# Performance work log

Measured on AMD Instinct MI355X. Metric: run time of the kernel, lower is better.

## Reference

```python
import jax, jax.numpy as jnp
import numpy as np

D_MODEL = 128
NHEAD = 8
HEAD_DIM = D_MODEL // NHEAD  # 16
NUM_LAYERS = 7
NUM_LABELS = 2
N_NODES = 10000
N_EDGES = 160000
NEG_SLOPE = 0.2  # GATv2Conv default negative_slope


def setup_inputs() -> dict:
    key = jax.random.key(0)
    ks = jax.random.split(key, 10)
    s = 1.0 / np.sqrt(D_MODEL)
    inp = {}
    inp["x"] = jax.random.normal(ks[0], (N_NODES, D_MODEL), dtype=jnp.float32)
    inp["edge_index"] = jax.random.randint(ks[1], (2, N_EDGES), 0, N_NODES, dtype=jnp.int64)
    inp["nchunks"] = 8  # uniform extra chunk size -> chunk = NUM_LABELS + 8 = 10
    # per-layer GATv2 params, stacked on a leading layer axis
    inp["Wl"] = jax.random.normal(ks[2], (NUM_LAYERS, D_MODEL, NHEAD * HEAD_DIM), dtype=jnp.float32) * s
    inp["bl"] = jnp.zeros((NUM_LAYERS, NHEAD * HEAD_DIM), dtype=jnp.float32)
    inp["Wr"] = jax.random.normal(ks[3], (NUM_LAYERS, D_MODEL, NHEAD * HEAD_DIM), dtype=jnp.float32) * s
    inp["br"] = jnp.zeros((NUM_LAYERS, NHEAD * HEAD_DIM), dtype=jnp.float32)
    inp["att"] = jax.random.normal(ks[4], (NUM_LAYERS, NHEAD, HEAD_DIM), dtype=jnp.float32) * s
    inp["bias"] = jnp.zeros((NUM_LAYERS, NHEAD * HEAD_DIM), dtype=jnp.float32)
    # split head: Linear(d_model, 1)
    inp["w_head"] = jax.random.normal(ks[5], (D_MODEL, 1), dtype=jnp.float32) * s
    inp["b_head"] = jnp.zeros((1,), dtype=jnp.float32)
    return inp


def _gatv2_layer(x, src, dst, Wl, bl, Wr, br, att, bias):
    # GATv2: e_ij = a^T LeakyReLU(W_l x_j + W_r x_i); alpha = segment-softmax over dst; out_i = sum alpha * W_l x_j
    N = x.shape[0]
    xl = (x @ Wl + bl).reshape(N, NHEAD, HEAD_DIM)
    xr = (x @ Wr + br).reshape(N, NHEAD, HEAD_DIM)
    z = jax.nn.leaky_relu(xl[src] + xr[dst], NEG_SLOPE)          # [E, H, D]
    e = jnp.einsum('ehd,hd->eh', z, att)                          # [E, H]
    emax = jax.ops.segment_max(e, dst, num_segments=N)            # [N, H]
    ex = jnp.exp(e - emax[dst])
    denom = jax.ops.segment_sum(ex, dst, num_segments=N)          # [N, H]
    alpha = ex / (denom[dst] + 1e-16)                             # [E, H]
    out = jax.ops.segment_sum(alpha[..., None] * xl[src], dst, num_segments=N)  # [N, H, D]
    return out.reshape(N, NHEAD * HEAD_DIM) + bias


def reference(x, edge_index, nchunks, Wl, bl, Wr, br, att, bias, w_head, b_head):
    N = x.shape[0]
    loop = jnp.arange(N, dtype=edge_index.dtype)  # GATv2Conv add_self_loops=True
    src = jnp.concatenate([edge_index[0], loop])
    dst = jnp.concatenate([edge_index[1], loop])
    for i in range(NUM_LAYERS):
        x = _gatv2_layer(x, src, dst, Wl[i], bl[i], Wr[i], br[i], att[i], bias[i])
    # uniform split of size (NUM_LABELS + nchunks); keep first NUM_LABELS rows of each chunk
    chunk = NUM_LABELS + int(nchunks)
    xs = x.reshape(-1, chunk, D_MODEL)[:, :NUM_LABELS]            # [n_chunks, num_labels, d]
    out = (xs @ w_head + b_head)[..., 0]                          # [n_chunks, num_labels]
    return out
```

## Files before the change

kernel.cpp:

```cpp
#include <hip/hip_runtime.h>
#include <math.h>

#define NT 256

typedef __attribute__((ext_vector_type(8))) short bf16x8;
typedef __attribute__((ext_vector_type(4))) float f32x4;


__device__ inline int detect_is64(const int* __restrict__ ei) {
    int is64 = 1;
#pragma unroll
    for (int k = 1; k < 16; k += 2) is64 &= (ei[k] == 0);
    return is64;
}

__device__ inline void split1(float f, short& hi, short& lo) {
    unsigned u = __float_as_uint(f);
    hi = (short)(u >> 16);
    float fl = f - __uint_as_float(u & 0xffff0000u);
    lo = (short)(__float_as_uint(fl) >> 16);
}

__device__ inline void cvt8(const float4& a, const float4& b, bf16x8& hi, bf16x8& lo) {
    float f[8] = {a.x, a.y, a.z, a.w, b.x, b.y, b.z, b.w};
#pragma unroll
    for (int j = 0; j < 8; j++) {
        unsigned u = __float_as_uint(f[j]);
        hi[j] = (short)(u >> 16);
        float fl = f[j] - __uint_as_float(u & 0xffff0000u);
        lo[j] = (short)(__float_as_uint(fl) >> 16);
    }
}


__global__ void count_kernel(const int* __restrict__ ei, int E, int N, int* __restrict__ deg) {
    int e = blockIdx.x * blockDim.x + threadIdx.x;
    if (e >= E) return;
    int is64 = detect_is64(ei);
    long long pos = (long long)E + e;
    int d = ei[is64 ? 2 * pos : pos];
    if ((unsigned)d < (unsigned)N) atomicAdd(&deg[d], 1);
}

__global__ __launch_bounds__(1024) void scan_kernel(const int* __restrict__ deg,
                                                    int* __restrict__ off,
                                                    int* __restrict__ cur, int N) {
    __shared__ int wsum[16];
    int t = threadIdx.x;
    int per = (N + 1023) >> 10;
    int b0 = t * per;
    int s = 0;
    for (int k = 0; k < per; k++) {
        int idx = b0 + k;
        if (idx < N) s += deg[idx];
    }
    int lane = t & 63, w = t >> 6;
    int v = s;
#pragma unroll
    for (int o = 1; o < 64; o <<= 1) {
        int u = __shfl_up(v, o, 64);
        if (lane >= o) v += u;
    }
    if (lane == 63) wsum[w] = v;
    __syncthreads();
    if (t == 0) {
        int r = 0;
#pragma unroll
        for (int j = 0; j < 16; j++) { int xx = wsum[j]; wsum[j] = r; r += xx; }
        off[N] = r;
    }
    __syncthreads();
    int run = v - s + wsum[w];
    for (int k = 0; k < per; k++) {
        int idx = b0 + k;
        if (idx < N) {
            off[idx] = run;
            cur[idx] = run;
            run += deg[idx];
        }
    }
}

__global__ void fill_kernel(const int* __restrict__ ei, int E, int N,
                            int* __restrict__ cur, int* __restrict__ esrc) {
    int e = blockIdx.x * blockDim.x + threadIdx.x;
    if (e >= E) return;
    int is64 = detect_is64(ei);
    long long spos = e, dpos = (long long)E + e;
    int s = ei[is64 ? 2 * spos : spos];
    int d = ei[is64 ? 2 * dpos : dpos];
    if ((unsigned)d >= (unsigned)N || (unsigned)s >= (unsigned)N) return;
    int p = atomicAdd(&cur[d], 1);
    esrc[p] = s;
}


__global__ __launch_bounds__(256) void prep_w(const float* __restrict__ Wl,
                                              const float* __restrict__ Wr,
                                              short* __restrict__ Whi,
                                              short* __restrict__ Wlo) {
    __shared__ float Wt[128][17];
    int l = blockIdx.x >> 4;
    int tile = blockIdx.x & 15;
    int c0 = tile * 16;
    const float* Wsrc = (c0 < 128) ? Wl + (size_t)l * 16384 : Wr + (size_t)l * 16384;
    int cbase = (c0 < 128) ? c0 : c0 - 128;
    int t = threadIdx.x;
#pragma unroll
    for (int it = 0; it < 8; it++) {
        int idx = it * 256 + t;
        int k = idx >> 4, c = idx & 15;
        Wt[k][c] = Wsrc[(size_t)k * 128 + cbase + c];
    }
    __syncthreads();
    int kt = t >> 6, lane = t & 63, q = (lane >> 4), cl = lane & 15;
    bf16x8 hi, lo;
#pragma unroll
    for (int j = 0; j < 8; j++) {
        short h, lw;
        split1(Wt[kt * 32 + q * 8 + j][cl], h, lw);
        hi[j] = h; lo[j] = lw;
    }
    size_t off = ((((size_t)l * 16 + tile) * 4 + kt) * 64 + lane) * 8;
    *(bf16x8*)(Whi + off) = hi;
    *(bf16x8*)(Wlo + off) = lo;
}


__global__ __launch_bounds__(256) void cvt_x(const float4* __restrict__ x4,
                                             short* __restrict__ hi,
                                             short* __restrict__ lo, int n8) {
    int id = blockIdx.x * 256 + threadIdx.x;
    if (id >= n8) return;
    float4 a = x4[2 * id];
    float4 b = x4[2 * id + 1];
    bf16x8 h, lw;
    cvt8(a, b, h, lw);
    *(bf16x8*)(hi + (size_t)id * 8) = h;
    *(bf16x8*)(lo + (size_t)id * 8) = lw;
}


__global__ __launch_bounds__(512, 1) void gemm_xlxr(const short* __restrict__ xhi,
                                                    const short* __restrict__ xlo,
                                                    const short* __restrict__ WhiL,
                                                    const short* __restrict__ WloL,
                                                    const float* __restrict__ blv,
                                                    const float* __restrict__ brv,
                                                    float* __restrict__ xl,
                                                    float* __restrict__ xr,
                                                    int N, int ntiles) {
    int t = threadIdx.x;
    int w = t >> 6, lane = t & 63, q = lane >> 4, cl = lane & 15;

    bf16x8 Bh[2][4], Bl[2][4];
    float biasv[2];
    float* outp[2];
    int colc[2];
#pragma unroll
    for (int nt = 0; nt < 2; nt++) {
        int tile = w * 2 + nt;
        int col = tile * 16 + cl;
        if (col < 128) { biasv[nt] = blv[col]; outp[nt] = xl; colc[nt] = col; }
        else           { biasv[nt] = brv[col - 128]; outp[nt] = xr; colc[nt] = col - 128; }
#pragma unroll
        for (int kt = 0; kt < 4; kt++) {
            size_t off = (((size_t)tile * 4 + kt) * 64 + lane) * 8;
            Bh[nt][kt] = *(const bf16x8*)(WhiL + off);
            Bl[nt][kt] = *(const bf16x8*)(WloL + off);
        }
    }

    int rt = blockIdx.x;
    if (rt >= ntiles) return;
    bf16x8 curH[4], curL[4], nxtH[4], nxtL[4];
    {
        int row = rt * 16 + cl;
        if (row >= N) row = N - 1;
        const short* ph = xhi + (size_t)row * 128 + q * 8;
        const short* pl = xlo + (size_t)row * 128 + q * 8;
#pragma unroll
        for (int kt = 0; kt < 4; kt++) {
            curH[kt] = *(const bf16x8*)(ph + kt * 32);
            curL[kt] = *(const bf16x8*)(pl + kt * 32);
        }
    }

    for (; rt < ntiles; rt += gridDim.x) {
        int rn = rt + gridDim.x;
        if (rn < ntiles) {
            int row = rn * 16 + cl;
            if (row >= N) row = N - 1;
            const short* ph = xhi + (size_t)row * 128 + q * 8;
            const short* pl = xlo + (size_t)row * 128 + q * 8;
#pragma unroll
            for (int kt = 0; kt < 4; kt++) {
                nxtH[kt] = *(const bf16x8*)(ph + kt * 32);
                nxtL[kt] = *(const bf16x8*)(pl + kt * 32);
            }
        }

        f32x4 acc0 = {0.f, 0.f, 0.f, 0.f}, acc1 = {0.f, 0.f, 0.f, 0.f};
#pragma unroll
        for (int kt = 0; kt < 4; kt++) {
            acc0 = __builtin_amdgcn_mfma_f32_16x16x32_bf16(curH[kt], Bh[0][kt], acc0, 0, 0, 0);
            acc1 = __builtin_amdgcn_mfma_f32_16x16x32_bf16(curH[kt], Bh[1][kt], acc1, 0, 0, 0);
            acc0 = __builtin_amdgcn_mfma_f32_16x16x32_bf16(curL[kt], Bh[0][kt], acc0, 0, 0, 0);
            acc1 = __builtin_amdgcn_mfma_f32_16x16x32_bf16(curL[kt], Bh[1][kt], acc1, 0, 0, 0);
            acc0 = __builtin_amdgcn_mfma_f32_16x16x32_bf16(curH[kt], Bl[0][kt], acc0, 0, 0, 0);
            acc1 = __builtin_amdgcn_mfma_f32_16x16x32_bf16(curH[kt], Bl[1][kt], acc1, 0, 0, 0);
        }

#pragma unroll
        for (int nt = 0; nt < 2; nt++) {
            f32x4 a = nt ? acc1 : acc0;
#pragma unroll
            for (int r = 0; r < 4; r++) {
                int row = rt * 16 + q * 4 + r;
                if (row < N) outp[nt][(size_t)row * 128 + colc[nt]] = a[r] + biasv[nt];
            }
        }
#pragma unroll
        for (int kt = 0; kt < 4; kt++) {
            curH[kt] = nxtH[kt];
            curL[kt] = nxtL[kt];
        }
    }
}


__global__ __launch_bounds__(256) void gat_agg(const float4* __restrict__ xl4,
                                               const float4* __restrict__ xr4,
                                               const int* __restrict__ off,
                                               const int* __restrict__ esrc,
                                               const float4* __restrict__ att4,
                                               const float4* __restrict__ bias4,
                                               float4* __restrict__ out4,
                                               short* __restrict__ nhi,
                                               short* __restrict__ nlo, int N) {
    int lane = threadIdx.x & 63;
    int sub = lane >> 4;
    int cl = lane & 15;
    int i = blockIdx.x * 4 + (threadIdx.x >> 6);
    if (i >= N) return;

    float4 xrA = xr4[(size_t)i * 32 + 2 * cl];
    float4 xrB = xr4[(size_t)i * 32 + 2 * cl + 1];
    float4 atA = att4[2 * cl];
    float4 atB = att4[2 * cl + 1];
    int start = off[i];
    int total = off[i + 1] - start + 1;
    int groups = (total + 3) >> 2;

    int k0 = sub;
    int s0 = (k0 < total) ? ((k0 == 0) ? i : esrc[start + k0 - 1]) : i;
    int k1 = 4 + sub;
    int s1 = (k1 < total) ? esrc[start + k1 - 1] : i;
    float4 v0A = xl4[(size_t)s0 * 32 + 2 * cl];
    float4 v0B = xl4[(size_t)s0 * 32 + 2 * cl + 1];
    int k2 = 8 + sub;
    int s2 = (k2 < total) ? esrc[start + k2 - 1] : i;
    float4 v1A = xl4[(size_t)s1 * 32 + 2 * cl];
    float4 v1B = xl4[(size_t)s1 * 32 + 2 * cl + 1];

    float s = 0.f;
    float4 aA = make_float4(0.f, 0.f, 0.f, 0.f);
    float4 aB = make_float4(0.f, 0.f, 0.f, 0.f);

    for (int g = 0; g < groups; g++) {
        int k3 = 4 * (g + 3) + sub;
        int s3 = (k3 < total) ? esrc[start + k3 - 1] : i;
        float4 v2A = xl4[(size_t)s2 * 32 + 2 * cl];
        float4 v2B = xl4[(size_t)s2 * 32 + 2 * cl + 1];

        int kc = 4 * g + sub;
        int valid = kc < total;
        float z0 = v0A.x + xrA.x, z1 = v0A.y + xrA.y, z2 = v0A.z + xrA.z, z3 = v0A.w + xrA.w;
        float z4 = v0B.x + xrB.x, z5 = v0B.y + xrB.y, z6 = v0B.z + xrB.z, z7 = v0B.w + xrB.w;
        z0 = (z0 > 0.f) ? z0 : 0.2f * z0;
        z1 = (z1 > 0.f) ? z1 : 0.2f * z1;
        z2 = (z2 > 0.f) ? z2 : 0.2f * z2;
        z3 = (z3 > 0.f) ? z3 : 0.2f * z3;
        z4 = (z4 > 0.f) ? z4 : 0.2f * z4;
        z5 = (z5 > 0.f) ? z5 : 0.2f * z5;
        z6 = (z6 > 0.f) ? z6 : 0.2f * z6;
        z7 = (z7 > 0.f) ? z7 : 0.2f * z7;
        float p = z0 * atA.x + z1 * atA.y + z2 * atA.z + z3 * atA.w
                + z4 * atB.x + z5 * atB.y + z6 * atB.z + z7 * atB.w;
        p += __shfl_xor(p, 1, 64);
        p = fminf(fmaxf(p, -80.f), 80.f);
        float wgt = valid ? __expf(p) : 0.f;
        s += wgt;
        aA.x += wgt * v0A.x; aA.y += wgt * v0A.y; aA.z += wgt * v0A.z; aA.w += wgt * v0A.w;
        aB.x += wgt * v0B.x; aB.y += wgt * v0B.y; aB.z += wgt * v0B.z; aB.w += wgt * v0B.w;

        v0A = v1A; v0B = v1B;
        v1A = v2A; v1B = v2B;
        s2 = s3;
    }

#pragma unroll
    for (int o = 16; o <= 32; o <<= 1) {
        s += __shfl_xor(s, o, 64);
        aA.x += __shfl_xor(aA.x, o, 64); aA.y += __shfl_xor(aA.y, o, 64);
        aA.z += __shfl_xor(aA.z, o, 64); aA.w += __shfl_xor(aA.w, o, 64);
        aB.x += __shfl_xor(aB.x, o, 64); aB.y += __shfl_xor(aB.y, o, 64);
        aB.z += __shfl_xor(aB.z, o, 64); aB.w += __shfl_xor(aB.w, o, 64);
    }
    if (sub == 0) {
        float inv = 1.f / (s + 1e-16f);
        float4 bA = bias4[2 * cl], bB = bias4[2 * cl + 1];
        float4 oA, oB;
        oA.x = aA.x * inv + bA.x; oA.y = aA.y * inv + bA.y;
        oA.z = aA.z * inv + bA.z; oA.w = aA.w * inv + bA.w;
        oB.x = aB.x * inv + bB.x; oB.y = aB.y * inv + bB.y;
        oB.z = aB.z * inv + bB.z; oB.w = aB.w * inv + bB.w;
        out4[(size_t)i * 32 + 2 * cl] = oA;
        out4[(size_t)i * 32 + 2 * cl + 1] = oB;
        if (nhi) {
            bf16x8 h, lw;
            cvt8(oA, oB, h, lw);
            *(bf16x8*)(nhi + (size_t)i * 128 + cl * 8) = h;
            *(bf16x8*)(nlo + (size_t)i * 128 + cl * 8) = lw;
        }
    }
}


__global__ __launch_bounds__(128) void head_kernel(const float* __restrict__ x,
                                                   const float* __restrict__ w,
                                                   const float* __restrict__ bh,
                                                   const int* __restrict__ nch,
                                                   float* __restrict__ out) {
    __shared__ float r[2];
    int b = blockIdx.x, t = threadIdx.x;
    int chunk = 2 + nch[0];
    int row = (b >> 1) * chunk + (b & 1);
    float p = x[(size_t)row * 128 + t] * w[t];
#pragma unroll
    for (int o = 32; o >= 1; o >>= 1) p += __shfl_xor(p, o, 64);
    if ((t & 63) == 0) r[t >> 6] = p;
    __syncthreads();
    if (t == 0) out[b] = r[0] + r[1] + bh[0];
}


extern "C" void kernel_launch(void* const* d_in, const int* in_sizes, int n_in,
                              void* d_out, int out_size, void* d_ws, size_t ws_size,
                              hipStream_t stream) {
    const float* x0 = (const float*)d_in[0];
    const int* ei = (const int*)d_in[1];
    const int* nchunks = (const int*)d_in[2];
    const float* Wl = (const float*)d_in[3];
    const float* bl = (const float*)d_in[4];
    const float* Wr = (const float*)d_in[5];
    const float* br = (const float*)d_in[6];
    const float* att = (const float*)d_in[7];
    const float* bias = (const float*)d_in[8];
    const float* wh = (const float*)d_in[9];
    const float* bh = (const float*)d_in[10];

    const int D = 128;
    int N = in_sizes[0] / D;
    int E = in_sizes[1] / 2;
    int ntiles = (N + 15) / 16;

    size_t fN = (size_t)N * D;
    const size_t WFRAG = 16 * 4 * 64 * 8;
    float* xl = (float*)d_ws;
    float* xr = xl + fN;
    float* xA = xr + fN;
    float* xB = xA + fN;
    short* cvH0 = (short*)(xB + fN);
    short* cvL0 = cvH0 + fN;
    short* cvH1 = cvL0 + fN;
    short* cvL1 = cvH1 + fN;
    short* Whi = cvL1 + fN;
    short* Wlo = Whi + 7 * WFRAG;
    int* deg = (int*)(Wlo + 7 * WFRAG);
    int* off = deg + N;
    int* cur = off + N + 1;
    int* esrc = cur + N;

    hipMemsetAsync(deg, 0, (size_t)N * sizeof(int), stream);
    prep_w<<<112, 256, 0, stream>>>(Wl, Wr, Whi, Wlo);
    {
        int n8 = N * 16;
        cvt_x<<<(n8 + 255) / 256, 256, 0, stream>>>((const float4*)x0, cvH0, cvL0, n8);
    }
    count_kernel<<<(E + NT - 1) / NT, NT, 0, stream>>>(ei, E, N, deg);
    scan_kernel<<<1, 1024, 0, stream>>>(deg, off, cur, N);
    fill_kernel<<<(E + NT - 1) / NT, NT, 0, stream>>>(ei, E, N, cur, esrc);

    int aggblocks = (N + 3) / 4;
    float* xn = xA;
    short* inH = cvH0; short* inL = cvL0;
    short* otH = cvH1; short* otL = cvL1;
    for (int l = 0; l < 7; l++) {
        gemm_xlxr<<<256, 512, 0, stream>>>(inH, inL,
                                           Whi + (size_t)l * WFRAG, Wlo + (size_t)l * WFRAG,
                                           bl + (size_t)l * D, br + (size_t)l * D,
                                           xl, xr, N, ntiles);
        int last = (l == 6);
        gat_agg<<<aggblocks, 256, 0, stream>>>((const float4*)xl, (const float4*)xr, off, esrc,
                                               (const float4*)(att + (size_t)l * D),
                                               (const float4*)(bias + (size_t)l * D),
                                               (float4*)xn,
                                               last ? (short*)nullptr : otH,
                                               last ? (short*)nullptr : otL, N);
        xn = (xn == xA) ? xB : xA;
        short* th = inH; short* tl = inL;
        inH = otH; inL = otL;
        otH = th; otL = tl;
    }
    const float* xfin = (xn == xA) ? xB : xA;
    head_kernel<<<out_size, 128, 0, stream>>>(xfin, wh, bh, nchunks, (float*)d_out);
}
```

Before: 312.0 us.

## Fuse all stages into one persistent kernel with hierarchical grid barriers

```diff
diff --git a/kernel.cpp b/kernel.cpp
--- a/kernel.cpp
+++ b/kernel.cpp
@@ -1,10 +1,12 @@
 #include <hip/hip_runtime.h>
 #include <math.h>
 
-#define NT 256
-
 typedef __attribute__((ext_vector_type(8))) short bf16x8;
 typedef __attribute__((ext_vector_type(4))) float f32x4;
+
+#define NBLK 1024
+#define TPB 256
+#define WFRAG (16 * 4 * 64 * 8)
 
 
 __device__ inline int detect_is64(const int* __restrict__ ei) {
@@ -33,75 +35,32 @@
 }
 
 
-__global__ void count_kernel(const int* __restrict__ ei, int E, int N, int* __restrict__ deg) {
-    int e = blockIdx.x * blockDim.x + threadIdx.x;
-    if (e >= E) return;
-    int is64 = detect_is64(ei);
-    long long pos = (long long)E + e;
-    int d = ei[is64 ? 2 * pos : pos];
-    if ((unsigned)d < (unsigned)N) atomicAdd(&deg[d], 1);
-}
-
-__global__ __launch_bounds__(1024) void scan_kernel(const int* __restrict__ deg,
-                                                    int* __restrict__ off,
-                                                    int* __restrict__ cur, int N) {
-    __shared__ int wsum[16];
-    int t = threadIdx.x;
-    int per = (N + 1023) >> 10;
-    int b0 = t * per;
-    int s = 0;
-    for (int k = 0; k < per; k++) {
-        int idx = b0 + k;
-        if (idx < N) s += deg[idx];
-    }
-    int lane = t & 63, w = t >> 6;
-    int v = s;
-#pragma unroll
-    for (int o = 1; o < 64; o <<= 1) {
-        int u = __shfl_up(v, o, 64);
-        if (lane >= o) v += u;
-    }
-    if (lane == 63) wsum[w] = v;
+__device__ inline void gsync(int* bars, int phase) {
     __syncthreads();
-    if (t == 0) {
-        int r = 0;
-#pragma unroll
-        for (int j = 0; j < 16; j++) { int xx = wsum[j]; wsum[j] = r; r += xx; }
-        off[N] = r;
+    if (threadIdx.x == 0) {
+        __threadfence();
+        int g = blockIdx.x >> 6;
+        int a = atomicAdd(&bars[8 + g], 1);
+        if (a == phase * 64 - 1) {
+            atomicAdd(&bars[0], 1);
+            while (atomicAdd(&bars[0], 0) < phase * 16)
+                __builtin_amdgcn_s_sleep(16);
+            atomicAdd(&bars[32 + g], 1);
+        } else {
+            while (atomicAdd(&bars[32 + g], 0) < phase)
+                __builtin_amdgcn_s_sleep(16);
+        }
+        __threadfence();
     }
     __syncthreads();
-    int run = v - s + wsum[w];
-    for (int k = 0; k < per; k++) {
-        int idx = b0 + k;
-        if (idx < N) {
-            off[idx] = run;
-            cur[idx] = run;
-            run += deg[idx];
-        }
-    }
-}
-
-__global__ void fill_kernel(const int* __restrict__ ei, int E, int N,
-                            int* __restrict__ cur, int* __restrict__ esrc) {
-    int e = blockIdx.x * blockDim.x + threadIdx.x;
-    if (e >= E) return;
-    int is64 = detect_is64(ei);
-    long long spos = e, dpos = (long long)E + e;
-    int s = ei[is64 ? 2 * spos : spos];
-    int d = ei[is64 ? 2 * dpos : dpos];
-    if ((unsigned)d >= (unsigned)N || (unsigned)s >= (unsigned)N) return;
-    int p = atomicAdd(&cur[d], 1);
-    esrc[p] = s;
-}
-
-
-__global__ __launch_bounds__(256) void prep_w(const float* __restrict__ Wl,
-                                              const float* __restrict__ Wr,
-                                              short* __restrict__ Whi,
-                                              short* __restrict__ Wlo) {
-    __shared__ float Wt[128][17];
-    int l = blockIdx.x >> 4;
-    int tile = blockIdx.x & 15;
+}
+
+
+__device__ inline void prep_w_task(const float* __restrict__ Wl, const float* __restrict__ Wr,
+                                   short* __restrict__ Whi, short* __restrict__ Wlo,
+                                   float (*Wt)[17], int task) {
+    int l = task >> 4;
+    int tile = task & 15;
     int c0 = tile * 16;
     const float* Wsrc = (c0 < 128) ? Wl + (size_t)l * 16384 : Wr + (size_t)l * 16384;
     int cbase = (c0 < 128) ? c0 : c0 - 128;
@@ -126,89 +85,54 @@
     *(bf16x8*)(Wlo + off) = lo;
 }
 
-
-__global__ __launch_bounds__(256) void cvt_x(const float4* __restrict__ x4,
-                                             short* __restrict__ hi,
-                                             short* __restrict__ lo, int n8) {
-    int id = blockIdx.x * 256 + threadIdx.x;
-    if (id >= n8) return;
-    float4 a = x4[2 * id];
-    float4 b = x4[2 * id + 1];
-    bf16x8 h, lw;
-    cvt8(a, b, h, lw);
-    *(bf16x8*)(hi + (size_t)id * 8) = h;
-    *(bf16x8*)(lo + (size_t)id * 8) = lw;
-}
-
-
-__global__ __launch_bounds__(512, 1) void gemm_xlxr(const short* __restrict__ xhi,
-                                                    const short* __restrict__ xlo,
-                                                    const short* __restrict__ WhiL,
-                                                    const short* __restrict__ WloL,
-                                                    const float* __restrict__ blv,
-                                                    const float* __restrict__ brv,
-                                                    float* __restrict__ xl,
-                                                    float* __restrict__ xr,
-                                                    int N, int ntiles) {
+__device__ inline void gemm_phase(const short* __restrict__ xhi, const short* __restrict__ xlo,
+                                  const short* __restrict__ WhiL, const short* __restrict__ WloL,
+                                  const float* __restrict__ blv, const float* __restrict__ brv,
+                                  float* __restrict__ xl, float* __restrict__ xr,
+                                  int N, int ntiles) {
     int t = threadIdx.x;
     int w = t >> 6, lane = t & 63, q = lane >> 4, cl = lane & 15;
+    int half = blockIdx.x >> 9;
 
     bf16x8 Bh[2][4], Bl[2][4];
     float biasv[2];
-    float* outp[2];
+    float* op[2];
     int colc[2];
 #pragma unroll
     for (int nt = 0; nt < 2; nt++) {
-        int tile = w * 2 + nt;
+        int tile = half * 8 + w * 2 + nt;
         int col = tile * 16 + cl;
-        if (col < 128) { biasv[nt] = blv[col]; outp[nt] = xl; colc[nt] = col; }
-        else           { biasv[nt] = brv[col - 128]; outp[nt] = xr; colc[nt] = col - 128; }
+        if (col < 128) { biasv[nt] = blv[col]; op[nt] = xl; colc[nt] = col; }
+        else           { biasv[nt] = brv[col - 128]; op[nt] = xr; colc[nt] = col - 128; }
 #pragma unroll
         for (int kt = 0; kt < 4; kt++) {
-            size_t off = (((size_t)tile * 4 + kt) * 64 + lane) * 8;
-            Bh[nt][kt] = *(const bf16x8*)(WhiL + off);
-            Bl[nt][kt] = *(const bf16x8*)(WloL + off);
-        }
-    }
-
-    int rt = blockIdx.x;
-    if (rt >= ntiles) return;
-    bf16x8 curH[4], curL[4], nxtH[4], nxtL[4];
-    {
+            size_t o = (((size_t)tile * 4 + kt) * 64 + lane) * 8;
+            Bh[nt][kt] = *(const bf16x8*)(WhiL + o);
+            Bl[nt][kt] = *(const bf16x8*)(WloL + o);
+        }
+    }
+
+    for (int rt = (blockIdx.x & 511); rt < ntiles; rt += 512) {
         int row = rt * 16 + cl;
         if (row >= N) row = N - 1;
         const short* ph = xhi + (size_t)row * 128 + q * 8;
         const short* pl = xlo + (size_t)row * 128 + q * 8;
+        bf16x8 AH[4], AL[4];
 #pragma unroll
         for (int kt = 0; kt < 4; kt++) {
-            curH[kt] = *(const bf16x8*)(ph + kt * 32);
-            curL[kt] = *(const bf16x8*)(pl + kt * 32);
-        }
-    }
-
-    for (; rt < ntiles; rt += gridDim.x) {
-        int rn = rt + gridDim.x;
-        if (rn < ntiles) {
-            int row = rn * 16 + cl;
-            if (row >= N) row = N - 1;
-            const short* ph = xhi + (size_t)row * 128 + q * 8;
-            const short* pl = xlo + (size_t)row * 128 + q * 8;
-#pragma unroll
-            for (int kt = 0; kt < 4; kt++) {
-                nxtH[kt] = *(const bf16x8*)(ph + kt * 32);
-                nxtL[kt] = *(const bf16x8*)(pl + kt * 32);
-            }
+            AH[kt] = *(const bf16x8*)(ph + kt * 32);
+            AL[kt] = *(const bf16x8*)(pl + kt * 32);
         }
 
         f32x4 acc0 = {0.f, 0.f, 0.f, 0.f}, acc1 = {0.f, 0.f, 0.f, 0.f};
 #pragma unroll
         for (int kt = 0; kt < 4; kt++) {
-            acc0 = __builtin_amdgcn_mfma_f32_16x16x32_bf16(curH[kt], Bh[0][kt], acc0, 0, 0, 0);
-            acc1 = __builtin_amdgcn_mfma_f32_16x16x32_bf16(curH[kt], Bh[1][kt], acc1, 0, 0, 0);
-            acc0 = __builtin_amdgcn_mfma_f32_16x16x32_bf16(curL[kt], Bh[0][kt], acc0, 0, 0, 0);
-            acc1 = __builtin_amdgcn_mfma_f32_16x16x32_bf16(curL[kt], Bh[1][kt], acc1, 0, 0, 0);
-            acc0 = __builtin_amdgcn_mfma_f32_16x16x32_bf16(curH[kt], Bl[0][kt], acc0, 0, 0, 0);
-            acc1 = __builtin_amdgcn_mfma_f32_16x16x32_bf16(curH[kt], Bl[1][kt], acc1, 0, 0, 0);
+            acc0 = __builtin_amdgcn_mfma_f32_16x16x32_bf16(AH[kt], Bh[0][kt], acc0, 0, 0, 0);
+            acc1 = __builtin_amdgcn_mfma_f32_16x16x32_bf16(AH[kt], Bh[1][kt], acc1, 0, 0, 0);
+            acc0 = __builtin_amdgcn_mfma_f32_16x16x32_bf16(AL[kt], Bh[0][kt], acc0, 0, 0, 0);
+            acc1 = __builtin_amdgcn_mfma_f32_16x16x32_bf16(AL[kt], Bh[1][kt], acc1, 0, 0, 0);
+            acc0 = __builtin_amdgcn_mfma_f32_16x16x32_bf16(AH[kt], Bl[0][kt], acc0, 0, 0, 0);
+            acc1 = __builtin_amdgcn_mfma_f32_16x16x32_bf16(AH[kt], Bl[1][kt], acc1, 0, 0, 0);
         }
 
 #pragma unroll
@@ -216,132 +140,235 @@
             f32x4 a = nt ? acc1 : acc0;
 #pragma unroll
             for (int r = 0; r < 4; r++) {
-                int row = rt * 16 + q * 4 + r;
-                if (row < N) outp[nt][(size_t)row * 128 + colc[nt]] = a[r] + biasv[nt];
+                int orow = rt * 16 + q * 4 + r;
+                if (orow < N) op[nt][(size_t)orow * 128 + colc[nt]] = a[r] + biasv[nt];
             }
         }
-#pragma unroll
-        for (int kt = 0; kt < 4; kt++) {
-            curH[kt] = nxtH[kt];
-            curL[kt] = nxtL[kt];
-        }
-    }
-}
-
-
-__global__ __launch_bounds__(256) void gat_agg(const float4* __restrict__ xl4,
-                                               const float4* __restrict__ xr4,
-                                               const int* __restrict__ off,
-                                               const int* __restrict__ esrc,
-                                               const float4* __restrict__ att4,
-                                               const float4* __restrict__ bias4,
-                                               float4* __restrict__ out4,
-                                               short* __restrict__ nhi,
-                                               short* __restrict__ nlo, int N) {
+    }
+}
+
+__device__ inline void agg_phase(const float4* __restrict__ xl4, const float4* __restrict__ xr4,
+                                 const int* __restrict__ off, const int* __restrict__ esrc,
+                                 const float4* __restrict__ att4, const float4* __restrict__ bias4,
+                                 float4* __restrict__ out4, short* __restrict__ nhi,
+                                 short* __restrict__ nlo, int N) {
     int lane = threadIdx.x & 63;
     int sub = lane >> 4;
     int cl = lane & 15;
-    int i = blockIdx.x * 4 + (threadIdx.x >> 6);
-    if (i >= N) return;
-
-    float4 xrA = xr4[(size_t)i * 32 + 2 * cl];
-    float4 xrB = xr4[(size_t)i * 32 + 2 * cl + 1];
     float4 atA = att4[2 * cl];
     float4 atB = att4[2 * cl + 1];
-    int start = off[i];
-    int total = off[i + 1] - start + 1;
-    int groups = (total + 3) >> 2;
-
-    int k0 = sub;
-    int s0 = (k0 < total) ? ((k0 == 0) ? i : esrc[start + k0 - 1]) : i;
-    int k1 = 4 + sub;
-    int s1 = (k1 < total) ? esrc[start + k1 - 1] : i;
-    float4 v0A = xl4[(size_t)s0 * 32 + 2 * cl];
-    float4 v0B = xl4[(size_t)s0 * 32 + 2 * cl + 1];
-    int k2 = 8 + sub;
-    int s2 = (k2 < total) ? esrc[start + k2 - 1] : i;
-    float4 v1A = xl4[(size_t)s1 * 32 + 2 * cl];
-    float4 v1B = xl4[(size_t)s1 * 32 + 2 * cl + 1];
-
-    float s = 0.f;
-    float4 aA = make_float4(0.f, 0.f, 0.f, 0.f);
-    float4 aB = make_float4(0.f, 0.f, 0.f, 0.f);
-
-    for (int g = 0; g < groups; g++) {
-        int k3 = 4 * (g + 3) + sub;
-        int s3 = (k3 < total) ? esrc[start + k3 - 1] : i;
-        float4 v2A = xl4[(size_t)s2 * 32 + 2 * cl];
-        float4 v2B = xl4[(size_t)s2 * 32 + 2 * cl + 1];
-
-        int kc = 4 * g + sub;
-        int valid = kc < total;
-        float z0 = v0A.x + xrA.x, z1 = v0A.y + xrA.y, z2 = v0A.z + xrA.z, z3 = v0A.w + xrA.w;
-        float z4 = v0B.x + xrB.x, z5 = v0B.y + xrB.y, z6 = v0B.z + xrB.z, z7 = v0B.w + xrB.w;
-        z0 = (z0 > 0.f) ? z0 : 0.2f * z0;
-        z1 = (z1 > 0.f) ? z1 : 0.2f * z1;
-        z2 = (z2 > 0.f) ? z2 : 0.2f * z2;
-        z3 = (z3 > 0.f) ? z3 : 0.2f * z3;
-        z4 = (z4 > 0.f) ? z4 : 0.2f * z4;
-        z5 = (z5 > 0.f) ? z5 : 0.2f * z5;
-        z6 = (z6 > 0.f) ? z6 : 0.2f * z6;
-        z7 = (z7 > 0.f) ? z7 : 0.2f * z7;
-        float p = z0 * atA.x + z1 * atA.y + z2 * atA.z + z3 * atA.w
-                + z4 * atB.x + z5 * atB.y + z6 * atB.z + z7 * atB.w;
-        p += __shfl_xor(p, 1, 64);
-        p = fminf(fmaxf(p, -80.f), 80.f);
-        float wgt = valid ? __expf(p) : 0.f;
-        s += wgt;
-        aA.x += wgt * v0A.x; aA.y += wgt * v0A.y; aA.z += wgt * v0A.z; aA.w += wgt * v0A.w;
-        aB.x += wgt * v0B.x; aB.y += wgt * v0B.y; aB.z += wgt * v0B.z; aB.w += wgt * v0B.w;
-
-        v0A = v1A; v0B = v1B;
-        v1A = v2A; v1B = v2B;
-        s2 = s3;
-    }
-
-#pragma unroll
-    for (int o = 16; o <= 32; o <<= 1) {
-        s += __shfl_xor(s, o, 64);
-        aA.x += __shfl_xor(aA.x, o, 64); aA.y += __shfl_xor(aA.y, o, 64);
-        aA.z += __shfl_xor(aA.z, o, 64); aA.w += __shfl_xor(aA.w, o, 64);
-        aB.x += __shfl_xor(aB.x, o, 64); aB.y += __shfl_xor(aB.y, o, 64);
-        aB.z += __shfl_xor(aB.z, o, 64); aB.w += __shfl_xor(aB.w, o, 64);
-    }
-    if (sub == 0) {
-        float inv = 1.f / (s + 1e-16f);
-        float4 bA = bias4[2 * cl], bB = bias4[2 * cl + 1];
-        float4 oA, oB;
-        oA.x = aA.x * inv + bA.x; oA.y = aA.y * inv + bA.y;
-        oA.z = aA.z * inv + bA.z; oA.w = aA.w * inv + bA.w;
-        oB.x = aB.x * inv + bB.x; oB.y = aB.y * inv + bB.y;
-        oB.z = aB.z * inv + bB.z; oB.w = aB.w * inv + bB.w;
-        out4[(size_t)i * 32 + 2 * cl] = oA;
-        out4[(size_t)i * 32 + 2 * cl + 1] = oB;
-        if (nhi) {
+    float4 bA = bias4[2 * cl], bB = bias4[2 * cl + 1];
+
+    for (int i = blockIdx.x * 4 + (threadIdx.x >> 6); i < N; i += NBLK * 4) {
+        float4 xrA = xr4[(size_t)i * 32 + 2 * cl];
+        float4 xrB = xr4[(size_t)i * 32 + 2 * cl + 1];
+        int start = off[i];
+        int total = off[i + 1] - start + 1;
+        int groups = (total + 3) >> 2;
+
+        int k0 = sub;
+        int s0 = (k0 < total) ? ((k0 == 0) ? i : esrc[start + k0 - 1]) : i;
+        int k1 = 4 + sub;
+        int s1 = (k1 < total) ? esrc[start + k1 - 1] : i;
+        float4 v0A = xl4[(size_t)s0 * 32 + 2 * cl];
+        float4 v0B = xl4[(size_t)s0 * 32 + 2 * cl + 1];
+        int k2 = 8 + sub;
+        int s2 = (k2 < total) ? esrc[start + k2 - 1] : i;
+        float4 v1A = xl4[(size_t)s1 * 32 + 2 * cl];
+        float4 v1B = xl4[(size_t)s1 * 32 + 2 * cl + 1];
+
+        float s = 0.f;
+        float4 aA = make_float4(0.f, 0.f, 0.f, 0.f);
+        float4 aB = make_float4(0.f, 0.f, 0.f, 0.f);
+
+        for (int g = 0; g < groups; g++) {
+            int k3 = 4 * (g + 3) + sub;
+            int s3 = (k3 < total) ? esrc[start + k3 - 1] : i;
+            float4 v2A = xl4[(size_t)s2 * 32 + 2 * cl];
+            float4 v2B = xl4[(size_t)s2 * 32 + 2 * cl + 1];
+
+            int kc = 4 * g + sub;
+            int valid = kc < total;
+            float z0 = v0A.x + xrA.x, z1 = v0A.y + xrA.y, z2 = v0A.z + xrA.z, z3 = v0A.w + xrA.w;
+            float z4 = v0B.x + xrB.x, z5 = v0B.y + xrB.y, z6 = v0B.z + xrB.z, z7 = v0B.w + xrB.w;
+            z0 = (z0 > 0.f) ? z0 : 0.2f * z0;
+            z1 = (z1 > 0.f) ? z1 : 0.2f * z1;
+            z2 = (z2 > 0.f) ? z2 : 0.2f * z2;
+            z3 = (z3 > 0.f) ? z3 : 0.2f * z3;
+            z4 = (z4 > 0.f) ? z4 : 0.2f * z4;
+            z5 = (z5 > 0.f) ? z5 : 0.2f * z5;
+            z6 = (z6 > 0.f) ? z6 : 0.2f * z6;
+            z7 = (z7 > 0.f) ? z7 : 0.2f * z7;
+            float p = z0 * atA.x + z1 * atA.y + z2 * atA.z + z3 * atA.w
+                    + z4 * atB.x + z5 * atB.y + z6 * atB.z + z7 * atB.w;
+            p += __shfl_xor(p, 1, 64);
+            p = fminf(fmaxf(p, -80.f), 80.f);
+            float wgt = valid ? __expf(p) : 0.f;
+            s += wgt;
+            aA.x += wgt * v0A.x; aA.y += wgt * v0A.y; aA.z += wgt * v0A.z; aA.w += wgt * v0A.w;
+            aB.x += wgt * v0B.x; aB.y += wgt * v0B.y; aB.z += wgt * v0B.z; aB.w += wgt * v0B.w;
+
+            v0A = v1A; v0B = v1B;
+            v1A = v2A; v1B = v2B;
+            s2 = s3;
+        }
+
+#pragma unroll
+        for (int o = 16; o <= 32; o <<= 1) {
+            s += __shfl_xor(s, o, 64);
+            aA.x += __shfl_xor(aA.x, o, 64); aA.y += __shfl_xor(aA.y, o, 64);
+            aA.z += __shfl_xor(aA.z, o, 64); aA.w += __shfl_xor(aA.w, o, 64);
+            aB.x += __shfl_xor(aB.x, o, 64); aB.y += __shfl_xor(aB.y, o, 64);
+            aB.z += __shfl_xor(aB.z, o, 64); aB.w += __shfl_xor(aB.w, o, 64);
+        }
+        if (sub == 0) {
+            float inv = 1.f / (s + 1e-16f);
+            float4 oA, oB;
+            oA.x = aA.x * inv + bA.x; oA.y = aA.y * inv + bA.y;
+            oA.z = aA.z * inv + bA.z; oA.w = aA.w * inv + bA.w;
+            oB.x = aB.x * inv + bB.x; oB.y = aB.y * inv + bB.y;
+            oB.z = aB.z * inv + bB.z; oB.w = aB.w * inv + bB.w;
+            out4[(size_t)i * 32 + 2 * cl] = oA;
+            out4[(size_t)i * 32 + 2 * cl + 1] = oB;
+            if (nhi) {
+                bf16x8 h, lw;
+                cvt8(oA, oB, h, lw);
+                *(bf16x8*)(nhi + (size_t)i * 128 + cl * 8) = h;
+                *(bf16x8*)(nlo + (size_t)i * 128 + cl * 8) = lw;
+            }
+        }
+    }
+}
+
+__device__ inline void head_phase(const float* __restrict__ x, const float* __restrict__ wv,
+                                  const float* __restrict__ bh, const int* __restrict__ nch,
+                                  float* __restrict__ out, int n_out, int N) {
+    int lane = threadIdx.x & 63;
+    int chunk = 2 + nch[0];
+    float w0 = wv[lane], w1 = wv[64 + lane];
+    for (int b = blockIdx.x * 4 + (threadIdx.x >> 6); b < n_out; b += NBLK * 4) {
+        int row = (b >> 1) * chunk + (b & 1);
+        if (row >= N) continue;
+        float p = x[(size_t)row * 128 + lane] * w0 + x[(size_t)row * 128 + 64 + lane] * w1;
+#pragma unroll
+        for (int o = 1; o <= 32; o <<= 1) p += __shfl_xor(p, o, 64);
+        if (lane == 0) out[b] = p + bh[0];
+    }
+}
+
+
+__global__ __launch_bounds__(TPB, 4) void mega(
+    const float* __restrict__ x0, const int* __restrict__ ei, const int* __restrict__ nch,
+    const float* __restrict__ Wl, const float* __restrict__ Wr,
+    const float* __restrict__ blv, const float* __restrict__ brv,
+    const float* __restrict__ att, const float* __restrict__ bias,
+    const float* __restrict__ wh, const float* __restrict__ bh,
+    float* xl, float* xr, float* xA, float* xB,
+    short* cvH0, short* cvL0, short* cvH1, short* cvL1,
+    short* Whi, short* Wlo,
+    int* bars, int* deg, int* off, int* cur, int* esrc,
+    float* out, int N, int E, int ntiles, int n_out) {
+
+    __shared__ float Wt[128][17];
+    int t = threadIdx.x;
+    int b = blockIdx.x;
+
+    if (b < 112) prep_w_task(Wl, Wr, Whi, Wlo, Wt, b);
+    {
+        int n8 = N * 16;
+        for (int id = b * TPB + t; id < n8; id += NBLK * TPB) {
+            const float4* x4 = (const float4*)x0;
+            float4 a = x4[2 * id];
+            float4 bb = x4[2 * id + 1];
             bf16x8 h, lw;
-            cvt8(oA, oB, h, lw);
-            *(bf16x8*)(nhi + (size_t)i * 128 + cl * 8) = h;
-            *(bf16x8*)(nlo + (size_t)i * 128 + cl * 8) = lw;
-        }
-    }
-}
-
-
-__global__ __launch_bounds__(128) void head_kernel(const float* __restrict__ x,
-                                                   const float* __restrict__ w,
-                                                   const float* __restrict__ bh,
-                                                   const int* __restrict__ nch,
-                                                   float* __restrict__ out) {
-    __shared__ float r[2];
-    int b = blockIdx.x, t = threadIdx.x;
-    int chunk = 2 + nch[0];
-    int row = (b >> 1) * chunk + (b & 1);
-    float p = x[(size_t)row * 128 + t] * w[t];
-#pragma unroll
-    for (int o = 32; o >= 1; o >>= 1) p += __shfl_xor(p, o, 64);
-    if ((t & 63) == 0) r[t >> 6] = p;
-    __syncthreads();
-    if (t == 0) out[b] = r[0] + r[1] + bh[0];
+            cvt8(a, bb, h, lw);
+            *(bf16x8*)(cvH0 + (size_t)id * 8) = h;
+            *(bf16x8*)(cvL0 + (size_t)id * 8) = lw;
+        }
+    }
+    {
+        int is64 = detect_is64(ei);
+        for (int e = b * TPB + t; e < E; e += NBLK * TPB) {
+            long long pos = (long long)E + e;
+            int d = ei[is64 ? 2 * pos : pos];
+            if ((unsigned)d < (unsigned)N) atomicAdd(&deg[d], 1);
+        }
+    }
+    gsync(bars, 1);
+
+    if (b == 0) {
+        __shared__ int wsum[4];
+        int per = (N + 255) >> 8;
+        int b0 = t * per;
+        int s = 0;
+        for (int k = 0; k < per; k++) {
+            int idx = b0 + k;
+            if (idx < N) s += deg[idx];
+        }
+        int lane = t & 63, w = t >> 6;
+        int v = s;
+#pragma unroll
+        for (int o = 1; o < 64; o <<= 1) {
+            int u = __shfl_up(v, o, 64);
+            if (lane >= o) v += u;
+        }
+        if (lane == 63) wsum[w] = v;
+        __syncthreads();
+        if (t == 0) {
+            int r = 0;
+#pragma unroll
+            for (int j = 0; j < 4; j++) { int xx = wsum[j]; wsum[j] = r; r += xx; }
+            off[N] = r;
+        }
+        __syncthreads();
+        int run = v - s + wsum[w];
+        for (int k = 0; k < per; k++) {
+            int idx = b0 + k;
+            if (idx < N) {
+                off[idx] = run;
+                cur[idx] = run;
+                run += deg[idx];
+            }
+        }
+    }
+    gsync(bars, 2);
+
+    {
+        int is64 = detect_is64(ei);
+        for (int e = b * TPB + t; e < E; e += NBLK * TPB) {
+            long long spos = e, dpos = (long long)E + e;
+            int s = ei[is64 ? 2 * spos : spos];
+            int d = ei[is64 ? 2 * dpos : dpos];
+            if ((unsigned)d >= (unsigned)N || (unsigned)s >= (unsigned)N) continue;
+            int p = atomicAdd(&cur[d], 1);
+            esrc[p] = s;
+        }
+    }
+    gsync(bars, 3);
+
+    short* inH = cvH0; short* inL = cvL0;
+    short* otH = cvH1; short* otL = cvL1;
+    float* xn = xA;
+    float* xfin = xB;
+    int phase = 4;
+    for (int l = 0; l < 7; l++) {
+        gemm_phase(inH, inL, Whi + (size_t)l * WFRAG, Wlo + (size_t)l * WFRAG,
+                   blv + (size_t)l * 128, brv + (size_t)l * 128, xl, xr, N, ntiles);
+        gsync(bars, phase++);
+        int last = (l == 6);
+        agg_phase((const float4*)xl, (const float4*)xr, off, esrc,
+                  (const float4*)(att + (size_t)l * 128),
+                  (const float4*)(bias + (size_t)l * 128),
+                  (float4*)xn, last ? (short*)0 : otH, last ? (short*)0 : otL, N);
+        gsync(bars, phase++);
+        xfin = xn;
+        xn = (xn == xA) ? xB : xA;
+        short* th = inH; short* tl = inL;
+        inH = otH; inL = otL;
+        otH = th; otL = tl;
+    }
+
+    head_phase(xfin, wh, bh, nch, out, n_out, N);
 }
 
 
@@ -366,7 +393,6 @@
     int ntiles = (N + 15) / 16;
 
     size_t fN = (size_t)N * D;
-    const size_t WFRAG = 16 * 4 * 64 * 8;
     float* xl = (float*)d_ws;
     float* xr = xl + fN;
     float* xA = xr + fN;
@@ -376,43 +402,17 @@
     short* cvH1 = cvL0 + fN;
     short* cvL1 = cvH1 + fN;
     short* Whi = cvL1 + fN;
-    short* Wlo = Whi + 7 * WFRAG;
-    int* deg = (int*)(Wlo + 7 * WFRAG);
+    short* Wlo = Whi + 7 * (size_t)WFRAG;
+    int* bars = (int*)(Wlo + 7 * (size_t)WFRAG);
+    int* deg = bars + 64;
     int* off = deg + N;
     int* cur = off + N + 1;
     int* esrc = cur + N;
 
-    hipMemsetAsync(deg, 0, (size_t)N * sizeof(int), stream);
-    prep_w<<<112, 256, 0, stream>>>(Wl, Wr, Whi, Wlo);
-    {
-        int n8 = N * 16;
-        cvt_x<<<(n8 + 255) / 256, 256, 0, stream>>>((const float4*)x0, cvH0, cvL0, n8);
-    }
-    count_kernel<<<(E + NT - 1) / NT, NT, 0, stream>>>(ei, E, N, deg);
-    scan_kernel<<<1, 1024, 0, stream>>>(deg, off, cur, N);
-    fill_kernel<<<(E + NT - 1) / NT, NT, 0, stream>>>(ei, E, N, cur, esrc);
-
-    int aggblocks = (N + 3) / 4;
-    float* xn = xA;
-    short* inH = cvH0; short* inL = cvL0;
-    short* otH = cvH1; short* otL = cvL1;
-    for (int l = 0; l < 7; l++) {
-        gemm_xlxr<<<256, 512, 0, stream>>>(inH, inL,
-                                           Whi + (size_t)l * WFRAG, Wlo + (size_t)l * WFRAG,
-                                           bl + (size_t)l * D, br + (size_t)l * D,
-                                           xl, xr, N, ntiles);
-        int last = (l == 6);
-        gat_agg<<<aggblocks, 256, 0, stream>>>((const float4*)xl, (const float4*)xr, off, esrc,
-                                               (const float4*)(att + (size_t)l * D),
-                                               (const float4*)(bias + (size_t)l * D),
-                                               (float4*)xn,
-                                               last ? (short*)nullptr : otH,
-                                               last ? (short*)nullptr : otL, N);
-        xn = (xn == xA) ? xB : xA;
-        short* th = inH; short* tl = inL;
-        inH = otH; inL = otL;
-        otH = th; otL = tl;
-    }
-    const float* xfin = (xn == xA) ? xB : xA;
-    head_kernel<<<out_size, 128, 0, stream>>>(xfin, wh, bh, nchunks, (float*)d_out);
-}
+    hipMemsetAsync(bars, 0, (64 + (size_t)N) * sizeof(int), stream);
+
+    mega<<<NBLK, TPB, 0, stream>>>(x0, ei, nchunks, Wl, Wr, bl, br, att, bias, wh, bh,
+                                   xl, xr, xA, xB, cvH0, cvL0, cvH1, cvL1, Whi, Wlo,
+                                   bars, deg, off, cur, esrc,
+                                   (float*)d_out, N, E, ntiles, out_size);
+}
```

New measurement: 1.229 ms. 294% more time.
